# Kernel optimization log

Measured on AMD Instinct MI355X. Metric: run time of the kernel, lower is better.

The kernel has to match this reference:

```python
import jax, jax.numpy as jnp
import numpy as np

EPS = 1e-7  # keras.backend.epsilon()
ROUTINGS = 3
NUM_CAPSULE = 32
DIM_CAPSULE = 64


def squash(x, axis=-1):
    # NOTE: faithful to the repo's (non-standard) squash: x / sqrt(||x||^2 + eps)
    s = jnp.sum(jnp.square(x), axis=axis, keepdims=True)
    return x / jnp.sqrt(s + EPS)


def setup_inputs() -> dict:
    key = jax.random.key(0)
    k1, k2 = jax.random.split(key)
    B, N_in, D_in = 64, 1024, 512
    u_vecs = jax.random.normal(k1, (B, N_in, D_in), dtype=jnp.float32)
    # shared capsule kernel: (1, input_dim, num_capsule * dim_capsule)
    W = jax.random.normal(k2, (1, D_in, NUM_CAPSULE * DIM_CAPSULE), dtype=jnp.float32) * (1.0 / np.sqrt(D_in))
    return {"u_vecs": u_vecs, "W": W}


def reference(u_vecs, W):
    B, N_in, D_in = u_vecs.shape
    # K.conv1d with a width-1 kernel == pointwise matmul
    u_hat = jnp.einsum('bid,dz->biz', u_vecs, W[0])  # [B, N_in, NC*DC]
    u_hat = u_hat.reshape(B, N_in, NUM_CAPSULE, DIM_CAPSULE)
    u_hat = jnp.transpose(u_hat, (0, 2, 1, 3))  # [B, NC, N_in, DC]

    b = jnp.zeros((B, NUM_CAPSULE, N_in), dtype=u_hat.dtype)
    outputs = None
    for i in range(ROUTINGS):
        # original permutes b to [B, N_in, NC] and softmaxes the last axis,
        # i.e. softmax over the output-capsule axis (axis=1 here)
        c = jax.nn.softmax(b, axis=1)  # [B, NC, N_in]
        outputs = squash(jnp.einsum('bni,bnid->bnd', c, u_hat))  # [B, NC, DC]
        if i < ROUTINGS - 1:
            b = jnp.einsum('bnd,bnid->bni', outputs, u_hat)  # agreement logits
    return outputs
```

## Files before the change

kernel.cpp:

```cpp
#include <hip/hip_runtime.h>

#define B_SZ   64
#define N_IN   1024
#define D_IN   512
#define NC     32
#define DC     64

typedef unsigned short u16;
typedef unsigned int   u32;
typedef __bf16 bf16x8 __attribute__((ext_vector_type(8)));
typedef unsigned short u16x8 __attribute__((ext_vector_type(8)));
typedef float f32x4  __attribute__((ext_vector_type(4)));
typedef float f32x16 __attribute__((ext_vector_type(16)));

__device__ __forceinline__ float bf2f(u16 u) {
    unsigned x = ((unsigned)u) << 16;
    return __builtin_bit_cast(float, x);
}
__device__ __forceinline__ u16 f2bf(float f) {
    unsigned x = __builtin_bit_cast(unsigned, f);
    unsigned r = (x + 0x7fffu + ((x >> 16) & 1u)) >> 16;
    return (u16)r;
}
__device__ __forceinline__ u16 f2h(float f) {
    return __builtin_bit_cast(u16, (_Float16)f);
}
__device__ __forceinline__ float h2f(u16 h) {
    return (float)__builtin_bit_cast(_Float16, h);
}

#define ASYNC_LDS16(g, l) __builtin_amdgcn_global_load_lds( \
    (const __attribute__((address_space(1))) void*)(g),     \
    (__attribute__((address_space(3))) void*)(l), 16, 0, 0)

__global__ __launch_bounds__(256) void w_conv(const float* __restrict__ W,
                                              u16* __restrict__ Wb) {
    const int i = blockIdx.x * 256 + threadIdx.x;
    float4 v = ((const float4*)W)[i];
    uint2 pk;
    pk.x = (u32)f2bf(v.x) | ((u32)f2bf(v.y) << 16);
    pk.y = (u32)f2bf(v.z) | ((u32)f2bf(v.w) << 16);
    ((uint2*)Wb)[i] = pk;
}

__global__ __launch_bounds__(256) void conv_rowsum(const float* __restrict__ A,
                                                   u16* __restrict__ Ab,
                                                   float* __restrict__ Arow) {
    const int tid = threadIdx.x;
    const int b  = blockIdx.x >> 3;
    const int r0 = (blockIdx.x & 7) << 7;
    const int q  = tid & 127;
    const int rh = tid >> 7;
    const size_t rowbase = (size_t)(b * N_IN + r0);
    float a0 = 0.f, a1 = 0.f, a2 = 0.f, a3 = 0.f;
    for (int r = rh; r < 128; r += 2) {
        float4 v = *(const float4*)(A + (rowbase + r) * 512 + q * 4);
        a0 += v.x; a1 += v.y; a2 += v.z; a3 += v.w;
        uint2 pk;
        pk.x = (u32)f2bf(v.x) | ((u32)f2bf(v.y) << 16);
        pk.y = (u32)f2bf(v.z) | ((u32)f2bf(v.w) << 16);
        *(uint2*)(Ab + (rowbase + r) * 512 + q * 4) = pk;
    }
    float* ar = Arow + b * 512 + q * 4;
    atomicAdd(ar + 0, a0);
    atomicAdd(ar + 1, a1);
    atomicAdd(ar + 2, a2);
    atomicAdd(ar + 3, a3);
}

__global__ __launch_bounds__(256) void s0_squash(const float* __restrict__ Arow,
                                                 const float* __restrict__ W,
                                                 float* __restrict__ outs) {
    const int tid = threadIdx.x;
    const int z   = blockIdx.x * 256 + tid;
    const int bg  = blockIdx.y * 4;
    float acc[4] = {};
    for (int k = 0; k < 512; ++k) {
        float wv = W[(size_t)k * 2048 + z];
#pragma unroll
        for (int bb = 0; bb < 4; ++bb)
            acc[bb] += Arow[(bg + bb) * 512 + k] * wv;
    }
#pragma unroll
    for (int bb = 0; bb < 4; ++bb) {
        float v = acc[bb] * 0.03125f;
        float sq = v * v;
        for (int off = 32; off; off >>= 1) sq += __shfl_xor(sq, off);
        outs[(size_t)(bg + bb) * 2048 + z] = v * (1.0f / sqrtf(sq + 1e-7f));
    }
}

__global__ __launch_bounds__(256) void g_pack(const u16* __restrict__ Wb,
                                              const float* __restrict__ outs,
                                              u16* __restrict__ Gpack) {
    __shared__ float vl[64 * 130];
    const int tid = threadIdx.x;
    const int kt  = blockIdx.x;
    const int np  = blockIdx.y;

    for (int t = tid; t < 8192; t += 256) {
        int b = t >> 7, idx = t & 127;
        vl[b * 130 + idx] = outs[(size_t)b * 2048 + np * 128 + idx];
    }
    __syncthreads();

    const int bs = tid & 15;
    const int k  = kt * 16 + (tid >> 4);
    float acc[4][2] = {};
    for (int n2 = 0; n2 < 2; ++n2) {
        const u16* wr = Wb + (size_t)k * 2048 + (np * 2 + n2) * 64;
        for (int d = 0; d < 64; ++d) {
            float wv = bf2f(wr[d]);
#pragma unroll
            for (int bb = 0; bb < 4; ++bb)
                acc[bb][n2] += wv * vl[(bs + 16 * bb) * 130 + n2 * 64 + d];
        }
    }
    const int kk = k >> 5, kq = k & 31;
#pragma unroll
    for (int bb = 0; bb < 4; ++bb)
#pragma unroll
        for (int n2 = 0; n2 < 2; ++n2) {
            int b = bs + 16 * bb, n = np * 2 + n2;
            Gpack[(((size_t)b * 16 + kk) * 32 + n) * 32 + kq] = f2bf(acc[bb][n2]);
        }
}

__global__ __launch_bounds__(256, 2) void routing_mfma(const u16* __restrict__ Ab,
                                                       const u16* __restrict__ Gpack,
                                                       u16* __restrict__ Mp) {
    __shared__ u16 Al[64 * 512];
    __shared__ u16 clb[64 * 34];
    const int tid   = threadIdx.x;
    const int lane  = tid & 63;
    const int w     = __builtin_amdgcn_readfirstlane(tid >> 6);
    const int b     = blockIdx.x >> 4;
    const int chunk = blockIdx.x & 15;
    const int row0  = chunk * 64;

    const size_t rowbase = (size_t)(b * N_IN + row0);
#pragma unroll
    for (int rr = 0; rr < 16; ++rr) {
        const int r   = w * 16 + rr;
        const int sig = (lane & 56) | ((lane & 7) ^ (r & 7));
        ASYNC_LDS16(Ab + (rowbase + r) * 512 + sig * 8, &Al[r * 512]);
    }
    __syncthreads();

    const int quad = lane >> 4;
    const int l16  = lane & 15;
    f32x4 lacc[2] = {};
    const u16* gb = Gpack + (size_t)b * 16384;
    {
        const int r  = w * 16 + l16;
        const u16* ar = &Al[r * 512];
        for (int kk = 0; kk < 16; ++kk) {
            const int c  = kk * 4 + quad;
            const int cs = (c & 56) | ((c & 7) ^ (r & 7));
            bf16x8 af = *(const bf16x8*)&ar[cs * 8];
#pragma unroll
            for (int nt = 0; nt < 2; ++nt) {
                bf16x8 bf = *(const bf16x8*)&gb[(kk * 32 + nt * 16 + l16) * 32 + quad * 8];
                lacc[nt] = __builtin_amdgcn_mfma_f32_16x16x32_bf16(af, bf, lacc[nt], 0, 0, 0);
            }
        }
    }

#pragma unroll
    for (int reg = 0; reg < 4; ++reg) {
        float m = fmaxf(lacc[0][reg], lacc[1][reg]);
        m = fmaxf(m, __shfl_xor(m, 1));
        m = fmaxf(m, __shfl_xor(m, 2));
        m = fmaxf(m, __shfl_xor(m, 4));
        m = fmaxf(m, __shfl_xor(m, 8));
        float e0 = __expf(lacc[0][reg] - m);
        float e1 = __expf(lacc[1][reg] - m);
        float s = e0 + e1;
        s += __shfl_xor(s, 1);
        s += __shfl_xor(s, 2);
        s += __shfl_xor(s, 4);
        s += __shfl_xor(s, 8);
        float inv = 1.f / s;
        const int row = w * 16 + quad * 4 + reg;
        clb[row * 34 + l16]      = f2bf(e0 * inv);
        clb[row * 34 + 16 + l16] = f2bf(e1 * inv);
    }
    __syncthreads();

    const int h   = lane >> 5;
    const int l32 = lane & 31;
    bf16x8 cfrag[4];
#pragma unroll
    for (int kk2 = 0; kk2 < 4; ++kk2) {
        u16x8 t;
#pragma unroll
        for (int j = 0; j < 8; ++j)
            t[j] = clb[(kk2 * 16 + h * 8 + j) * 34 + l32];
        cfrag[kk2] = __builtin_bit_cast(bf16x8, t);
    }
    u16* mpb = Mp + ((size_t)b * 16 + chunk) * 32 * 512;
    for (int cti = 0; cti < 4; ++cti) {
        const int ct   = w * 4 + cti;
        const int kcol = ct * 32 + l32;
        const int c2   = kcol >> 3;
        const int e    = kcol & 7;
        f32x16 acc = {};
#pragma unroll
        for (int kk2 = 0; kk2 < 4; ++kk2) {
            u16x8 t;
#pragma unroll
            for (int j = 0; j < 8; ++j) {
                const int r2  = kk2 * 16 + h * 8 + j;
                const int cs2 = (c2 & 56) | ((c2 & 7) ^ (r2 & 7));
                t[j] = Al[r2 * 512 + cs2 * 8 + e];
            }
            bf16x8 bf = __builtin_bit_cast(bf16x8, t);
            acc = __builtin_amdgcn_mfma_f32_32x32x16_bf16(cfrag[kk2], bf, acc, 0, 0, 0);
        }
#pragma unroll
        for (int reg = 0; reg < 16; ++reg) {
            const int n = (reg & 3) + 8 * (reg >> 2) + 4 * h;
            mpb[(size_t)n * 512 + kcol] = f2h(acc[reg]);
        }
    }
}

__global__ __launch_bounds__(256, 2) void s_final(const u16* __restrict__ Mp,
                                                  const u16* __restrict__ Wb,
                                                  float* __restrict__ outs,
                                                  float* __restrict__ outf) {
    __shared__ u16   Wl[512 * 64];
    __shared__ float Ml[8 * 512];
    const int tid = threadIdx.x;
    const int n   = blockIdx.x;
    const int bg  = blockIdx.y * 8;

    for (int t = tid; t < 8192; t += 256) {
        int k = t >> 4, d4 = t & 15;
        ((uint2*)Wl)[t] = *(const uint2*)(Wb + (size_t)k * 2048 + n * 64 + d4 * 4);
    }
    for (int t = tid; t < 2048; t += 256) {
        int bs = t >> 8, kp = t & 255;
        const u32* p = (const u32*)(Mp + (((size_t)(bg + bs) * 16) * 32 + n) * 512) + kp;
        float s0 = 0.f, s1 = 0.f;
#pragma unroll
        for (int ch = 0; ch < 16; ++ch) {
            u32 v = p[(size_t)ch * 32 * 256];
            s0 += h2f((u16)(v & 0xffffu));
            s1 += h2f((u16)(v >> 16));
        }
        Ml[bs * 512 + kp * 2]     = s0;
        Ml[bs * 512 + kp * 2 + 1] = s1;
    }
    __syncthreads();

    const int w = tid >> 6;
    const int d = tid & 63;
    float acc[2] = {};
    for (int k = 0; k < 512; ++k) {
        float wv = bf2f(Wl[k * 64 + d]);
        acc[0] += Ml[(w * 2) * 512 + k] * wv;
        acc[1] += Ml[(w * 2 + 1) * 512 + k] * wv;
    }
#pragma unroll
    for (int i = 0; i < 2; ++i) {
        const int b = bg + w * 2 + i;
        float sq = acc[i] * acc[i];
        for (int off = 32; off; off >>= 1) sq += __shfl_xor(sq, off);
        float o = acc[i] * (1.0f / sqrtf(sq + 1e-7f));
        size_t idx = (size_t)b * 2048 + n * 64 + d;
        outs[idx] = o;
        if (outf) outf[idx] = o;
    }
}

extern "C" void kernel_launch(void* const* d_in, const int* in_sizes, int n_in,
                              void* d_out, int out_size, void* d_ws, size_t ws_size,
                              hipStream_t stream) {
    (void)in_sizes; (void)n_in; (void)out_size; (void)ws_size;
    const float* A = (const float*)d_in[0];
    const float* W = (const float*)d_in[1];
    float* out     = (float*)d_out;

    uint8_t* ws = (uint8_t*)d_ws;
    const size_t AB_B    = (size_t)B_SZ * N_IN * D_IN * 2;
    const size_t AROW_B  = (size_t)B_SZ * D_IN * 4;
    const size_t OUTS_B  = (size_t)B_SZ * NC * DC * 4;
    const size_t GP_B    = (size_t)B_SZ * 16 * 32 * 32 * 2;
    const size_t WB_B    = (size_t)D_IN * NC * DC * 2;
    u16*   Ab    = (u16*)ws;
    float* Arow  = (float*)(ws + AB_B);
    float* outs  = (float*)(ws + AB_B + AROW_B);
    u16*   Gpack = (u16*)(ws + AB_B + AROW_B + OUTS_B);
    u16*   Wb    = (u16*)(ws + AB_B + AROW_B + OUTS_B + GP_B);
    u16*   Mp    = (u16*)(ws + AB_B + AROW_B + OUTS_B + GP_B + WB_B);

    w_conv<<<1024, 256, 0, stream>>>(W, Wb);
    hipMemsetAsync(Arow, 0, AROW_B, stream);
    conv_rowsum<<<512, 256, 0, stream>>>(A, Ab, Arow);

    s0_squash<<<dim3(8, 16), 256, 0, stream>>>(Arow, W, outs);

    for (int it = 0; it < 2; ++it) {
        g_pack<<<dim3(32, 16), 256, 0, stream>>>(Wb, outs, Gpack);
        routing_mfma<<<1024, 256, 0, stream>>>(Ab, Gpack, Mp);
        s_final<<<dim3(32, 8), 256, 0, stream>>>(Mp, Wb, outs, it == 1 ? out : nullptr);
    }
}
```

Baseline: 383.9 us.

## Fuse conversion kernels, replace atomics with partial rowsums, vectorize g_pack

Merges the W bf16 conversion and the A conversion/rowsum into a single launch. The memset and atomic accumulation are replaced by per-slot partial rowsums, which s0_squash reduces into shared memory. s0_squash now reads bf16 W and uses a finer batch grid. g_pack reads W in 8-wide vectors and uses a padded LDS stride for vector loads. This removes two launches, the memset and the atomics, at the cost of a larger workspace and an extra reduction pass.

```diff
diff --git a/kernel.cpp b/kernel.cpp
--- a/kernel.cpp
+++ b/kernel.cpp
@@ -33,27 +33,32 @@
     (const __attribute__((address_space(1))) void*)(g),     \
     (__attribute__((address_space(3))) void*)(l), 16, 0, 0)
 
-__global__ __launch_bounds__(256) void w_conv(const float* __restrict__ W,
-                                              u16* __restrict__ Wb) {
-    const int i = blockIdx.x * 256 + threadIdx.x;
-    float4 v = ((const float4*)W)[i];
-    uint2 pk;
-    pk.x = (u32)f2bf(v.x) | ((u32)f2bf(v.y) << 16);
-    pk.y = (u32)f2bf(v.z) | ((u32)f2bf(v.w) << 16);
-    ((uint2*)Wb)[i] = pk;
-}
-
-__global__ __launch_bounds__(256) void conv_rowsum(const float* __restrict__ A,
-                                                   u16* __restrict__ Ab,
-                                                   float* __restrict__ Arow) {
+__global__ __launch_bounds__(256) void conv_all(const float* __restrict__ A,
+                                                const float* __restrict__ W,
+                                                u16* __restrict__ Ab,
+                                                u16* __restrict__ Wb,
+                                                float* __restrict__ Arowp) {
     const int tid = threadIdx.x;
-    const int b  = blockIdx.x >> 3;
-    const int r0 = (blockIdx.x & 7) << 7;
+    if (blockIdx.x >= 1024) {
+        const int wb = blockIdx.x - 1024;
+#pragma unroll
+        for (int it = 0; it < 16; ++it) {
+            int i = wb * 4096 + it * 256 + tid;
+            float4 v = ((const float4*)W)[i];
+            uint2 pk;
+            pk.x = (u32)f2bf(v.x) | ((u32)f2bf(v.y) << 16);
+            pk.y = (u32)f2bf(v.z) | ((u32)f2bf(v.w) << 16);
+            ((uint2*)Wb)[i] = pk;
+        }
+        return;
+    }
+    const int b  = blockIdx.x >> 4;
+    const int r0 = (blockIdx.x & 15) << 6;
     const int q  = tid & 127;
     const int rh = tid >> 7;
     const size_t rowbase = (size_t)(b * N_IN + r0);
     float a0 = 0.f, a1 = 0.f, a2 = 0.f, a3 = 0.f;
-    for (int r = rh; r < 128; r += 2) {
+    for (int r = rh; r < 64; r += 2) {
         float4 v = *(const float4*)(A + (rowbase + r) * 512 + q * 4);
         a0 += v.x; a1 += v.y; a2 += v.z; a3 += v.w;
         uint2 pk;
@@ -61,28 +66,37 @@
         pk.y = (u32)f2bf(v.z) | ((u32)f2bf(v.w) << 16);
         *(uint2*)(Ab + (rowbase + r) * 512 + q * 4) = pk;
     }
-    float* ar = Arow + b * 512 + q * 4;
-    atomicAdd(ar + 0, a0);
-    atomicAdd(ar + 1, a1);
-    atomicAdd(ar + 2, a2);
-    atomicAdd(ar + 3, a3);
-}
-
-__global__ __launch_bounds__(256) void s0_squash(const float* __restrict__ Arow,
-                                                 const float* __restrict__ W,
+    const int slot = (blockIdx.x & 15) * 2 + rh;
+    float* ar = Arowp + ((size_t)b * 32 + slot) * 512 + q * 4;
+    ar[0] = a0; ar[1] = a1; ar[2] = a2; ar[3] = a3;
+}
+
+__global__ __launch_bounds__(256) void s0_squash(const float* __restrict__ Arowp,
+                                                 const u16* __restrict__ Wb,
                                                  float* __restrict__ outs) {
+    __shared__ float Al[2 * 512];
     const int tid = threadIdx.x;
     const int z   = blockIdx.x * 256 + tid;
-    const int bg  = blockIdx.y * 4;
-    float acc[4] = {};
+    const int bg  = blockIdx.y * 2;
+
+    for (int t = tid; t < 1024; t += 256) {
+        int bb = t >> 9, k = t & 511;
+        const float* p = Arowp + ((size_t)(bg + bb) * 32) * 512 + k;
+        float s = 0.f;
+#pragma unroll
+        for (int j = 0; j < 32; ++j) s += p[(size_t)j * 512];
+        Al[t] = s;
+    }
+    __syncthreads();
+
+    float acc[2] = {};
     for (int k = 0; k < 512; ++k) {
-        float wv = W[(size_t)k * 2048 + z];
-#pragma unroll
-        for (int bb = 0; bb < 4; ++bb)
-            acc[bb] += Arow[(bg + bb) * 512 + k] * wv;
-    }
-#pragma unroll
-    for (int bb = 0; bb < 4; ++bb) {
+        float wv = bf2f(Wb[(size_t)k * 2048 + z]);
+        acc[0] += Al[k] * wv;
+        acc[1] += Al[512 + k] * wv;
+    }
+#pragma unroll
+    for (int bb = 0; bb < 2; ++bb) {
         float v = acc[bb] * 0.03125f;
         float sq = v * v;
         for (int off = 32; off; off >>= 1) sq += __shfl_xor(sq, off);
@@ -93,27 +107,40 @@
 __global__ __launch_bounds__(256) void g_pack(const u16* __restrict__ Wb,
                                               const float* __restrict__ outs,
                                               u16* __restrict__ Gpack) {
-    __shared__ float vl[64 * 130];
+    __shared__ float vl[64 * 132];
     const int tid = threadIdx.x;
     const int kt  = blockIdx.x;
     const int np  = blockIdx.y;
 
     for (int t = tid; t < 8192; t += 256) {
         int b = t >> 7, idx = t & 127;
-        vl[b * 130 + idx] = outs[(size_t)b * 2048 + np * 128 + idx];
+        vl[b * 132 + idx] = outs[(size_t)b * 2048 + np * 128 + idx];
     }
     __syncthreads();
 
     const int bs = tid & 15;
     const int k  = kt * 16 + (tid >> 4);
     float acc[4][2] = {};
+#pragma unroll
     for (int n2 = 0; n2 < 2; ++n2) {
         const u16* wr = Wb + (size_t)k * 2048 + (np * 2 + n2) * 64;
-        for (int d = 0; d < 64; ++d) {
-            float wv = bf2f(wr[d]);
-#pragma unroll
-            for (int bb = 0; bb < 4; ++bb)
-                acc[bb][n2] += wv * vl[(bs + 16 * bb) * 130 + n2 * 64 + d];
+#pragma unroll
+        for (int d8 = 0; d8 < 8; ++d8) {
+            u16x8 w8 = *(const u16x8*)&wr[d8 * 8];
+            float wf[8];
+#pragma unroll
+            for (int j = 0; j < 8; ++j) wf[j] = bf2f(w8[j]);
+#pragma unroll
+            for (int bb = 0; bb < 4; ++bb) {
+                const float* vp = &vl[(bs + 16 * bb) * 132 + n2 * 64 + d8 * 8];
+                f32x4 va = *(const f32x4*)vp;
+                f32x4 vb = *(const f32x4*)(vp + 4);
+#pragma unroll
+                for (int j = 0; j < 4; ++j) {
+                    acc[bb][n2] += wf[j]     * va[j];
+                    acc[bb][n2] += wf[j + 4] * vb[j];
+                }
+            }
         }
     }
     const int kk = k >> 5, kq = k & 31;
@@ -284,22 +311,20 @@
 
     uint8_t* ws = (uint8_t*)d_ws;
     const size_t AB_B    = (size_t)B_SZ * N_IN * D_IN * 2;
-    const size_t AROW_B  = (size_t)B_SZ * D_IN * 4;
+    const size_t AROWP_B = (size_t)B_SZ * 32 * D_IN * 4;
     const size_t OUTS_B  = (size_t)B_SZ * NC * DC * 4;
     const size_t GP_B    = (size_t)B_SZ * 16 * 32 * 32 * 2;
     const size_t WB_B    = (size_t)D_IN * NC * DC * 2;
     u16*   Ab    = (u16*)ws;
-    float* Arow  = (float*)(ws + AB_B);
-    float* outs  = (float*)(ws + AB_B + AROW_B);
-    u16*   Gpack = (u16*)(ws + AB_B + AROW_B + OUTS_B);
-    u16*   Wb    = (u16*)(ws + AB_B + AROW_B + OUTS_B + GP_B);
-    u16*   Mp    = (u16*)(ws + AB_B + AROW_B + OUTS_B + GP_B + WB_B);
-
-    w_conv<<<1024, 256, 0, stream>>>(W, Wb);
-    hipMemsetAsync(Arow, 0, AROW_B, stream);
-    conv_rowsum<<<512, 256, 0, stream>>>(A, Ab, Arow);
-
-    s0_squash<<<dim3(8, 16), 256, 0, stream>>>(Arow, W, outs);
+    float* Arowp = (float*)(ws + AB_B);
+    float* outs  = (float*)(ws + AB_B + AROWP_B);
+    u16*   Gpack = (u16*)(ws + AB_B + AROWP_B + OUTS_B);
+    u16*   Wb    = (u16*)(ws + AB_B + AROWP_B + OUTS_B + GP_B);
+    u16*   Mp    = (u16*)(ws + AB_B + AROWP_B + OUTS_B + GP_B + WB_B);
+
+    conv_all<<<1088, 256, 0, stream>>>(A, W, Ab, Wb, Arowp);
+
+    s0_squash<<<dim3(8, 32), 256, 0, stream>>>(Arowp, Wb, outs);
 
     for (int it = 0; it < 2; ++it) {
         g_pack<<<dim3(32, 16), 256, 0, stream>>>(Wb, outs, Gpack);
```

New measurement: 370.7 us. 1.04x faster.
